# Performance work log

Hardware: AMD Instinct MI355X
Metric: run time of the kernel (lower is better)

## Reference

```python
import math
import jax, jax.numpy as jnp
import numpy as np

DIM = 96
HEADS = 3
HEAD_DIM = DIM // HEADS
WS = 8            # window_size
SHIFT = 4         # shift_size
N = WS * WS       # tokens per window
SCALE = HEAD_DIM ** (-0.5)


def _relative_positions_log():
    # matches WindowAttention.get_relative_positions (torch.meshgrid ij)
    coords = jnp.stack(jnp.meshgrid(jnp.arange(WS), jnp.arange(WS), indexing='ij'))  # [2,WS,WS]
    flat = coords.reshape(2, -1)                                # [2,N]
    rel = flat[:, :, None] - flat[:, None, :]                   # [2,N,N]
    rel = jnp.transpose(rel, (1, 2, 0)).astype(jnp.float32)     # [N,N,2]
    return jnp.sign(rel) * jnp.log1p(jnp.abs(rel))


def _conv1x1(x, w, b):
    # x: [B,C,H,W], w: [O,C], b: [O]
    return jnp.einsum('bchw,oc->bohw', x, w) + b[:, None, None]


def _conv3x3_reflect(x, w, b):
    # reflect padding=1, kernel 3x3
    xp = jnp.pad(x, ((0, 0), (0, 0), (1, 1), (1, 1)), mode='reflect')
    y = jax.lax.conv_general_dilated(xp, w, (1, 1), 'VALID',
                                     dimension_numbers=('NCHW', 'OIHW', 'NCHW'))
    return y + b[None, :, None, None]


def setup_inputs() -> dict:
    key = jax.random.key(0)
    ks = jax.random.split(key, 16)
    s = 0.02
    inp = {
        'x':      jax.random.normal(ks[0], (8, DIM, 256, 256), jnp.float32),
        'V_w':    jax.random.normal(ks[1], (DIM, DIM), jnp.float32) * s,
        'V_b':    jnp.zeros((DIM,), jnp.float32),
        'QK_w':   jax.random.normal(ks[2], (2 * DIM, DIM), jnp.float32) * s,
        'QK_b':   jnp.zeros((2 * DIM,), jnp.float32),
        'conv_w': jax.random.normal(ks[3], (DIM, DIM, 3, 3), jnp.float32) * s,
        'conv_b': jnp.zeros((DIM,), jnp.float32),
        'proj_w': jax.random.normal(ks[4], (DIM, DIM), jnp.float32) * s,
        'proj_b': jnp.zeros((DIM,), jnp.float32),
        'm1_w':   jax.random.normal(ks[5], (256, 2), jnp.float32) * 0.1,
        'm1_b':   jnp.zeros((256,), jnp.float32),
        'm2_w':   jax.random.normal(ks[6], (HEADS, 256), jnp.float32) * 0.1,
        'm2_b':   jnp.zeros((HEADS,), jnp.float32),
    }
    return inp


def reference(x, V_w, V_b, QK_w, QK_b, conv_w, conv_b, proj_w, proj_b,
              m1_w, m1_b, m2_w, m2_b):
    B, C, H, W = x.shape
    V = _conv1x1(x, V_w, V_b)                     # [B,C,H,W]
    QK = _conv1x1(x, QK_w, QK_b)                  # [B,2C,H,W]
    QKV = jnp.concatenate([QK, V], axis=1)        # [B,3C,H,W]

    # check_size with shift: H,W divisible by WS -> mod_pad = 0
    pad_r = (WS - SHIFT) % WS
    QKV = jnp.pad(QKV, ((0, 0), (0, 0), (SHIFT, pad_r), (SHIFT, pad_r)), mode='reflect')
    Ht, Wt = QKV.shape[2], QKV.shape[3]

    # window partition -> [B*nH*nW, N, 3C]
    sQ = jnp.transpose(QKV, (0, 2, 3, 1))         # [B,Ht,Wt,3C]
    nH, nW = Ht // WS, Wt // WS
    qkv = sQ.reshape(B, nH, WS, nW, WS, 3 * C)
    qkv = jnp.transpose(qkv, (0, 1, 3, 2, 4, 5)).reshape(-1, N, 3 * C)

    # window attention with MLP relative-position bias
    Bw = qkv.shape[0]
    qkv = qkv.reshape(Bw, N, 3, HEADS, HEAD_DIM)
    qkv = jnp.transpose(qkv, (2, 0, 3, 1, 4))     # [3,Bw,h,N,d]
    q, k, v = qkv[0], qkv[1], qkv[2]

    rel = _relative_positions_log()               # [N,N,2]
    hbias = jax.nn.gelu(rel @ m1_w.T + m1_b, approximate=False)
    bias = hbias @ m2_w.T + m2_b                  # [N,N,h]
    bias = jnp.transpose(bias, (2, 0, 1))         # [h,N,N]

    attn = jnp.einsum('bhnd,bhmd->bhnm', q, k) * SCALE + bias[None]
    attn = jax.nn.softmax(attn, axis=-1)
    xw = jnp.einsum('bhnm,bhmd->bhnd', attn, v)   # [Bw,h,N,d]
    xw = jnp.transpose(xw, (0, 2, 1, 3)).reshape(Bw, N, C)

    # window reverse -> [B,Ht,Wt,C]
    xr = xw.reshape(B, nH, nW, WS, WS, C)
    xr = jnp.transpose(xr, (0, 1, 3, 2, 4, 5)).reshape(B, Ht, Wt, C)
    attn_out = xr[:, SHIFT:SHIFT + H, SHIFT:SHIFT + W, :]
    attn_out = jnp.transpose(attn_out, (0, 3, 1, 2))   # [B,C,H,W]

    conv_out = _conv3x3_reflect(V, conv_w, conv_b)
    x_out = _conv1x1(conv_out + attn_out, proj_w, proj_b)
    return x_out
```

## Files before the change

kernel.cpp:

```cpp
#include <hip/hip_runtime.h>
#include <cstdint>

using u16 = unsigned short;
using u32 = unsigned int;
using f32x4  = __attribute__((ext_vector_type(4))) float;
using bf16x8 = __attribute__((ext_vector_type(8))) short;

#define NHEADS 3
#define WSZ 8
#define IMG 256
#define NPX 65536
#define NWIN 33
#define ATT_SCALE 0.17677669529663687f
#define INV_SCALE 5.656854249492381f
#define HALO_PITCH 104

__device__ __forceinline__ int refl(int i, int n) {
    return i < 0 ? -i : (i >= n ? 2*n - 2 - i : i);
}
__device__ __forceinline__ float bflo(u32 u){ union{u32 i; float f;} x; x.i = u << 16; return x.f; }
__device__ __forceinline__ float bfhi(u32 u){ union{u32 i; float f;} x; x.i = u & 0xffff0000u; return x.f; }
__device__ __forceinline__ float bf2f(u16 v){ union{u32 i; float f;} x; x.i = ((u32)v) << 16; return x.f; }
__device__ __forceinline__ u16 f2bf(float f){
    union{float f; u32 i;} x; x.f = f;
    u32 r = x.i + 0x7fffu + ((x.i >> 16) & 1u);
    return (u16)(r >> 16);
}
__device__ __forceinline__ u32 pk2bf(float a, float b){
    return (u32)f2bf(a) | ((u32)f2bf(b) << 16);
}

__global__ __launch_bounds__(256) void k_bias(
    const float* __restrict__ m1w, const float* __restrict__ m1b,
    const float* __restrict__ m2w, const float* __restrict__ m2b,
    float* __restrict__ biasS)
{
    int idx = blockIdx.x * 256 + threadIdx.x;
    int hh  = idx >> 12;
    int rem = idx & 4095;
    int n = rem >> 6, m = rem & 63;
    int di = (n >> 3) - (m >> 3);
    int dj = (n & 7)  - (m & 7);
    float fdi = copysignf(log1pf(fabsf((float)di)), (float)di);
    float fdj = copysignf(log1pf(fabsf((float)dj)), (float)dj);
    float acc = m2b[hh];
    for (int k = 0; k < 256; ++k) {
        float tv = fdi * m1w[2*k] + fdj * m1w[2*k+1] + m1b[k];
        float g  = 0.5f * tv * (1.0f + erff(tv * 0.70710678118654752f));
        acc = fmaf(g, m2w[hh*256 + k], acc);
    }
    biasS[hh*4096 + n*64 + m] = acc * INV_SCALE;
}

__global__ __launch_bounds__(64) void k_wprep(
    const float* __restrict__ cw, u16* __restrict__ Bfrag)
{
    int ks   = blockIdx.x;
    int lane = threadIdx.x;
    int nt    = ks % 6;
    int kstep = ks / 6;
    int tap   = kstep % 9;
    int ck    = kstep / 9;
    int dy = tap / 3, dx = tap % 3;
    int cout = nt*16 + (lane & 15);
    int cin0 = ck*32 + (lane >> 4)*8;
    u16* dst = Bfrag + (size_t)ks*512 + lane*8;
    #pragma unroll
    for (int j = 0; j < 8; ++j)
        dst[j] = f2bf(cw[((size_t)(cout*96 + cin0 + j))*9 + dy*3 + dx]);
}

__global__ __launch_bounds__(64) void k_wprep_qkv(
    const float* __restrict__ qkw, const float* __restrict__ vw,
    u16* __restrict__ BfragQ)
{
    int ks   = blockIdx.x;
    int lane = threadIdx.x;
    int nt    = ks % 18;
    int kstep = ks / 18;
    int o     = nt*16 + (lane & 15);
    int cin0  = kstep*32 + (lane >> 4)*8;
    const float* src = (o < 192) ? (qkw + (size_t)o*96 + cin0)
                                 : (vw + (size_t)(o - 192)*96 + cin0);
    u16* dst = BfragQ + (size_t)ks*512 + lane*8;
    #pragma unroll
    for (int j = 0; j < 8; ++j) dst[j] = f2bf(src[j]);
}

__global__ __launch_bounds__(64) void k_wprep_proj(
    const float* __restrict__ pw, u16* __restrict__ BfragP)
{
    int ks   = blockIdx.x;
    int lane = threadIdx.x;
    int nt    = ks % 6;
    int kstep = ks / 6;
    int o     = nt*16 + (lane & 15);
    int cin0  = kstep*32 + (lane >> 4)*8;
    u16* dst = BfragP + (size_t)ks*512 + lane*8;
    #pragma unroll
    for (int j = 0; j < 8; ++j) dst[j] = f2bf(pw[(size_t)o*96 + cin0 + j]);
}

__global__ __launch_bounds__(256, 2) void k_qkv(
    const float* __restrict__ x, const u16* __restrict__ BfragQ,
    const float* __restrict__ qkb, const float* __restrict__ vb,
    u16* __restrict__ qkv)
{
    int tile = blockIdx.x;
    int b    = tile >> 8;
    int pix0 = (tile & 255) * 256;
    size_t px0 = (size_t)tile * 256;
    int t    = threadIdx.x;

    __shared__ u16 xs[256 * HALO_PITCH];

    {
        const float* xb = x + (size_t)b*96*NPX + pix0 + t;
        u16* xrow = xs + t * HALO_PITCH;
        float v[96];
        #pragma unroll
        for (int c = 0; c < 96; ++c) v[c] = xb[(size_t)c * NPX];
        #pragma unroll
        for (int oct = 0; oct < 12; ++oct) {
            uint4 o;
            o.x = pk2bf(v[oct*8+0], v[oct*8+1]);
            o.y = pk2bf(v[oct*8+2], v[oct*8+3]);
            o.z = pk2bf(v[oct*8+4], v[oct*8+5]);
            o.w = pk2bf(v[oct*8+6], v[oct*8+7]);
            *(uint4*)(xrow + oct*8) = o;
        }
    }
    __syncthreads();

    int wv   = __builtin_amdgcn_readfirstlane(t >> 6);
    int lane = t & 63;
    int lc   = lane & 15;
    int kg   = lane >> 4;

    const u16* bbase = BfragQ + lane*8;

    #pragma unroll 1
    for (int og = 0; og < 3; ++og) {
        f32x4 acc[4][6] = {};
        #pragma unroll
        for (int kstep = 0; kstep < 3; ++kstep) {
            bf16x8 bF[6];
            #pragma unroll
            for (int nt = 0; nt < 6; ++nt)
                bF[nt] = *(const bf16x8*)(bbase + (size_t)(kstep*18 + og*6 + nt)*512);
            #pragma unroll
            for (int mt = 0; mt < 4; ++mt) {
                bf16x8 aF = *(const bf16x8*)(xs + (wv*64 + mt*16 + lc)*HALO_PITCH + kstep*32 + kg*8);
                #pragma unroll
                for (int nt = 0; nt < 6; ++nt)
                    acc[mt][nt] = __builtin_amdgcn_mfma_f32_16x16x32_bf16(aF, bF[nt], acc[mt][nt], 0, 0, 0);
            }
        }

        float bv[6];
        #pragma unroll
        for (int nt = 0; nt < 6; ++nt) {
            int o = og*96 + nt*16 + lc;
            bv[nt] = (o < 192) ? qkb[o] : vb[o - 192];
        }

        #pragma unroll
        for (int mt = 0; mt < 4; ++mt) {
            #pragma unroll
            for (int r = 0; r < 4; ++r) {
                size_t px = px0 + wv*64 + mt*16 + kg*4 + r;
                u16* qp = qkv + px*288 + og*96 + lc;
                #pragma unroll
                for (int nt = 0; nt < 6; ++nt)
                    qp[nt*16] = f2bf(acc[mt][nt][r] + bv[nt]);
            }
        }
    }
}

__global__ __launch_bounds__(256, 2) void k_attn(
    const u16* __restrict__ qkv, const float* __restrict__ biasS,
    u16* __restrict__ att)
{
    __shared__ u16 lds[27648];
    int t    = threadIdx.x;
    int wv   = __builtin_amdgcn_readfirstlane(t >> 6);
    int lane = t & 63;
    int lc   = lane & 15;
    int kg   = lane >> 4;

    u16* Plds = lds + wv * 6912;
    u16* Vlds = Plds + 4608;

    int win = blockIdx.x * 4 + wv;
    int b   = win / 1089;
    int wr  = win - b * 1089;
    int wy  = wr / NWIN;
    int wx  = wr - wy * NWIN;

    int py = wy*8 + (lane >> 3) - 4;
    int px = wx*8 + (lane & 7)  - 4;
    int iy = refl(py, IMG), ix = refl(px, IMG);
    int pxoff = b*NPX + iy*256 + ix;
    int vpx = (py >= 0 && py < IMG && px >= 0 && px < IMG) ? pxoff : (int)(pxoff | 0x80000000u);

    int pxA[4];
    #pragma unroll
    for (int mt = 0; mt < 4; ++mt)
        pxA[mt] = __builtin_amdgcn_ds_bpermute((16*mt + lc)*4, vpx) & 0x7fffffff;

    #pragma unroll 1
    for (int h = 0; h < 3; ++h) {
        {
            const u16* vrow = qkv + (size_t)pxoff*288 + 192 + h*32;
            #pragma unroll
            for (int g = 0; g < 4; ++g) {
                bf16x8 vv = *(const bf16x8*)(vrow + g*8);
                #pragma unroll
                for (int j = 0; j < 8; ++j)
                    Vlds[(g*8 + j)*72 + lane] = (u16)vv[j];
            }
        }

        bf16x8 afr[4], bfr[4];
        #pragma unroll
        for (int mt = 0; mt < 4; ++mt) {
            afr[mt] = *(const bf16x8*)(qkv + (size_t)pxA[mt]*288 + 96 + h*32 + kg*8);
            bfr[mt] = *(const bf16x8*)(qkv + (size_t)pxA[mt]*288 +      h*32 + kg*8);
        }

        f32x4 acc[4][4];
        const float* bb = biasS + h*4096 + lc*64 + 4*kg;
        #pragma unroll
        for (int nt = 0; nt < 4; ++nt)
            #pragma unroll
            for (int mt = 0; mt < 4; ++mt)
                acc[mt][nt] = *(const f32x4*)(bb + nt*1024 + mt*16);

        #pragma unroll
        for (int mt = 0; mt < 4; ++mt)
            #pragma unroll
            for (int nt = 0; nt < 4; ++nt)
                acc[mt][nt] = __builtin_amdgcn_mfma_f32_16x16x32_bf16(afr[mt], bfr[nt], acc[mt][nt], 0, 0, 0);

        #pragma unroll
        for (int nt = 0; nt < 4; ++nt) {
            float m = acc[0][nt][0];
            #pragma unroll
            for (int mt = 0; mt < 4; ++mt)
                #pragma unroll
                for (int r = 0; r < 4; ++r)
                    m = fmaxf(m, acc[mt][nt][r]);
            m = fmaxf(m, __shfl_xor(m, 16));
            m = fmaxf(m, __shfl_xor(m, 32));
            float s = 0.f;
            #pragma unroll
            for (int mt = 0; mt < 4; ++mt)
                #pragma unroll
                for (int r = 0; r < 4; ++r) {
                    float p = __expf((acc[mt][nt][r] - m) * ATT_SCALE);
                    acc[mt][nt][r] = p;
                    s += p;
                }
            s += __shfl_xor(s, 16);
            s += __shfl_xor(s, 32);
            float inv = 1.0f / s;
            #pragma unroll
            for (int mt = 0; mt < 4; ++mt)
                #pragma unroll
                for (int r = 0; r < 4; ++r)
                    acc[mt][nt][r] *= inv;
        }

        #pragma unroll
        for (int nt = 0; nt < 4; ++nt)
            #pragma unroll
            for (int mt = 0; mt < 4; ++mt) {
                uint2 pk;
                pk.x = pk2bf(acc[mt][nt][0], acc[mt][nt][1]);
                pk.y = pk2bf(acc[mt][nt][2], acc[mt][nt][3]);
                *(uint2*)(Plds + (16*nt + lc)*72 + 16*mt + 4*kg) = pk;
            }

        f32x4 oacc[4][2] = {};
        #pragma unroll
        for (int s = 0; s < 2; ++s) {
            bf16x8 vb2[2];
            #pragma unroll
            for (int ntpv = 0; ntpv < 2; ++ntpv)
                vb2[ntpv] = *(const bf16x8*)(Vlds + (16*ntpv + lc)*72 + s*32 + kg*8);
            #pragma unroll
            for (int mtpv = 0; mtpv < 4; ++mtpv) {
                bf16x8 pa = *(const bf16x8*)(Plds + (16*mtpv + lc)*72 + s*32 + kg*8);
                #pragma unroll
                for (int ntpv = 0; ntpv < 2; ++ntpv)
                    oacc[mtpv][ntpv] = __builtin_amdgcn_mfma_f32_16x16x32_bf16(pa, vb2[ntpv], oacc[mtpv][ntpv], 0, 0, 0);
            }
        }

        #pragma unroll
        for (int mtpv = 0; mtpv < 4; ++mtpv)
            #pragma unroll
            for (int rr = 0; rr < 4; ++rr) {
                int vp = __builtin_amdgcn_ds_bpermute((16*mtpv + 4*kg + rr)*4, vpx);
                if (vp >= 0) {
                    u16* op = att + (size_t)vp*96 + h*32 + lc;
                    op[0]  = f2bf(oacc[mtpv][0][rr]);
                    op[16] = f2bf(oacc[mtpv][1][rr]);
                }
            }
    }
}

__global__ __launch_bounds__(256, 2) void k_conv(
    const u16* __restrict__ qkv, const u16* __restrict__ att,
    const u16* __restrict__ Bfrag, const float* __restrict__ cb,
    u16* __restrict__ S)
{
    int tile = blockIdx.x;
    int b    = tile >> 8;
    int tr   = tile & 255;
    int ty0  = (tr >> 3) * 8;
    int tx0  = (tr & 7) * 32;
    int t    = threadIdx.x;

    __shared__ u16 vt[340 * HALO_PITCH];

    for (int p = t; p < 340; p += 256) {
        int hr = p / 34;
        int hc = p - hr * 34;
        int gy = refl(ty0 - 1 + hr, IMG);
        int gx = refl(tx0 - 1 + hc, IMG);
        const uint4* src = (const uint4*)(qkv + ((size_t)(b*NPX + gy*256 + gx))*288 + 192);
        uint4* dst = (uint4*)(vt + p * HALO_PITCH);
        #pragma unroll
        for (int q = 0; q < 12; ++q) dst[q] = src[q];
    }
    __syncthreads();

    int wv   = __builtin_amdgcn_readfirstlane(t >> 6);
    int lane = t & 63;
    int lc   = lane & 15;
    int kg   = lane >> 4;

    int abase[4];
    #pragma unroll
    for (int mt = 0; mt < 4; ++mt) {
        int r_mt = 2*wv + (mt >> 1);
        int c_mt = (mt & 1) * 16;
        abase[mt] = (r_mt*34 + c_mt + lc) * HALO_PITCH + kg*8;
    }

    f32x4 acc[4][6] = {};

    const u16* bfr = Bfrag + lane*8;
    #pragma unroll 1
    for (int ck = 0; ck < 3; ++ck) {
        const u16* bck = bfr + ck * 27648;
        int aoff = ck * 32;
        #pragma unroll
        for (int tap = 0; tap < 9; ++tap) {
            const int dy = tap / 3, dx = tap % 3;
            bf16x8 bF[6];
            #pragma unroll
            for (int nt = 0; nt < 6; ++nt)
                bF[nt] = *(const bf16x8*)(bck + (tap*6 + nt)*512);
            #pragma unroll
            for (int mt = 0; mt < 4; ++mt) {
                bf16x8 aF = *(const bf16x8*)(vt + abase[mt] + aoff + (dy*34 + dx)*HALO_PITCH);
                #pragma unroll
                for (int nt = 0; nt < 6; ++nt)
                    acc[mt][nt] = __builtin_amdgcn_mfma_f32_16x16x32_bf16(aF, bF[nt], acc[mt][nt], 0, 0, 0);
            }
        }
    }

    float cbv[6];
    #pragma unroll
    for (int nt = 0; nt < 6; ++nt) cbv[nt] = cb[nt*16 + lc];

    #pragma unroll
    for (int mt = 0; mt < 4; ++mt) {
        int r_mt = 2*wv + (mt >> 1);
        int c_mt = (mt & 1) * 16;
        int y    = ty0 + r_mt;
        #pragma unroll
        for (int r = 0; r < 4; ++r) {
            int x = tx0 + c_mt + kg*4 + r;
            size_t pbase = ((size_t)(b*NPX + y*256 + x))*96 + lc;
            #pragma unroll
            for (int nt = 0; nt < 6; ++nt) {
                float v = acc[mt][nt][r] + cbv[nt] + bf2f(att[pbase + nt*16]);
                S[pbase + nt*16] = f2bf(v);
            }
        }
    }
}

__global__ __launch_bounds__(256, 2) void k_proj(
    const u16* __restrict__ S, const u16* __restrict__ BfragP,
    const float* __restrict__ pb, float* __restrict__ out)
{
    int tile = blockIdx.x;
    int b    = tile >> 8;
    int pix0 = (tile & 255) * 256;
    size_t px0 = (size_t)tile * 256;
    int t    = threadIdx.x;
    int wv   = __builtin_amdgcn_readfirstlane(t >> 6);
    int lane = t & 63;
    int lc   = lane & 15;
    int kg   = lane >> 4;

    f32x4 acc[4][6] = {};
    const u16* arow  = S + (px0 + wv*64 + lc)*96 + kg*8;
    const u16* bbase = BfragP + lane*8;

    #pragma unroll
    for (int kstep = 0; kstep < 3; ++kstep) {
        bf16x8 bF[6];
        #pragma unroll
        for (int nt = 0; nt < 6; ++nt)
            bF[nt] = *(const bf16x8*)(bbase + (size_t)(kstep*6 + nt)*512);
        #pragma unroll
        for (int mt = 0; mt < 4; ++mt) {
            bf16x8 aF = *(const bf16x8*)(arow + (size_t)mt*16*96 + kstep*32);
            #pragma unroll
            for (int nt = 0; nt < 6; ++nt)
                acc[mt][nt] = __builtin_amdgcn_mfma_f32_16x16x32_bf16(aF, bF[nt], acc[mt][nt], 0, 0, 0);
        }
    }

    float bv[6];
    #pragma unroll
    for (int nt = 0; nt < 6; ++nt) bv[nt] = pb[nt*16 + lc];

    float* ob = out + (size_t)b*96*NPX;
    #pragma unroll
    for (int mt = 0; mt < 4; ++mt) {
        #pragma unroll
        for (int r = 0; r < 4; ++r) {
            int pxi = pix0 + wv*64 + mt*16 + kg*4 + r;
            #pragma unroll
            for (int nt = 0; nt < 6; ++nt)
                ob[(size_t)(nt*16 + lc)*NPX + pxi] = acc[mt][nt][r] + bv[nt];
        }
    }
}

extern "C" void kernel_launch(void* const* d_in, const int* in_sizes, int n_in,
                              void* d_out, int out_size, void* d_ws, size_t ws_size,
                              hipStream_t stream)
{
    const float* x      = (const float*)d_in[0];
    const float* V_w    = (const float*)d_in[1];
    const float* V_b    = (const float*)d_in[2];
    const float* QK_w   = (const float*)d_in[3];
    const float* QK_b   = (const float*)d_in[4];
    const float* conv_w = (const float*)d_in[5];
    const float* conv_b = (const float*)d_in[6];
    const float* proj_w = (const float*)d_in[7];
    const float* proj_b = (const float*)d_in[8];
    const float* m1_w   = (const float*)d_in[9];
    const float* m1_b   = (const float*)d_in[10];
    const float* m2_w   = (const float*)d_in[11];
    const float* m2_b   = (const float*)d_in[12];
    float* out = (float*)d_out;

    char* ws = (char*)d_ws;
    float* biasS = (float*)ws;
    u16* qkvb = (u16*)(ws + 49152);
    u16* attb = (u16*)(ws + 49152 + 301989888);
    u16* sbuf = (u16*)(ws + 49152 + 301989888 + 100663296);

    char* ob = (char*)d_out;
    u16* Bfrag  = (u16*)ob;
    u16* BfragQ = (u16*)(ob + (1 << 20));
    u16* BfragP = (u16*)attb;

    hipLaunchKernelGGL(k_wprep,      dim3(162),     dim3(64),  0, stream, conv_w, Bfrag);
    hipLaunchKernelGGL(k_wprep_qkv,  dim3(54),      dim3(64),  0, stream, QK_w, V_w, BfragQ);
    hipLaunchKernelGGL(k_bias,       dim3(48),      dim3(256), 0, stream, m1_w, m1_b, m2_w, m2_b, biasS);
    hipLaunchKernelGGL(k_qkv,        dim3(2048),    dim3(256), 0, stream, x, BfragQ, QK_b, V_b, qkvb);
    hipLaunchKernelGGL(k_attn,       dim3(2178),    dim3(256), 0, stream, qkvb, biasS, attb);
    hipLaunchKernelGGL(k_conv,       dim3(2048),    dim3(256), 0, stream, qkvb, attb, Bfrag, conv_b, sbuf);
    hipLaunchKernelGGL(k_wprep_proj, dim3(18),      dim3(64),  0, stream, proj_w, BfragP);
    hipLaunchKernelGGL(k_proj,       dim3(2048),    dim3(256), 0, stream, sbuf, BfragP, proj_b, out);
}
```

Before: 591.7 us.

## Fuse 3x3 conv and 1x1 projection into one kernel via LDS staging

After: 523.8 us. -11.5%, faster.

```diff
diff --git a/kernel.cpp b/kernel.cpp
--- a/kernel.cpp
+++ b/kernel.cpp
@@ -312,10 +312,11 @@
     }
 }
 
-__global__ __launch_bounds__(256, 2) void k_conv(
+__global__ __launch_bounds__(256, 2) void k_convproj(
     const u16* __restrict__ qkv, const u16* __restrict__ att,
     const u16* __restrict__ Bfrag, const float* __restrict__ cb,
-    u16* __restrict__ S)
+    const u16* __restrict__ BfragP, const float* __restrict__ pb,
+    float* __restrict__ out)
 {
     int tile = blockIdx.x;
     int b    = tile >> 8;
@@ -379,6 +380,8 @@
     #pragma unroll
     for (int nt = 0; nt < 6; ++nt) cbv[nt] = cb[nt*16 + lc];
 
+    __syncthreads();
+
     #pragma unroll
     for (int mt = 0; mt < 4; ++mt) {
         int r_mt = 2*wv + (mt >> 1);
@@ -386,35 +389,21 @@
         int y    = ty0 + r_mt;
         #pragma unroll
         for (int r = 0; r < 4; ++r) {
-            int x = tx0 + c_mt + kg*4 + r;
+            int x  = tx0 + c_mt + kg*4 + r;
+            int pl = r_mt*32 + c_mt + kg*4 + r;
             size_t pbase = ((size_t)(b*NPX + y*256 + x))*96 + lc;
+            u16* srow = vt + pl * HALO_PITCH + lc;
             #pragma unroll
             for (int nt = 0; nt < 6; ++nt) {
                 float v = acc[mt][nt][r] + cbv[nt] + bf2f(att[pbase + nt*16]);
-                S[pbase + nt*16] = f2bf(v);
-            }
-        }
-    }
-}
-
-__global__ __launch_bounds__(256, 2) void k_proj(
-    const u16* __restrict__ S, const u16* __restrict__ BfragP,
-    const float* __restrict__ pb, float* __restrict__ out)
-{
-    int tile = blockIdx.x;
-    int b    = tile >> 8;
-    int pix0 = (tile & 255) * 256;
-    size_t px0 = (size_t)tile * 256;
-    int t    = threadIdx.x;
-    int wv   = __builtin_amdgcn_readfirstlane(t >> 6);
-    int lane = t & 63;
-    int lc   = lane & 15;
-    int kg   = lane >> 4;
-
-    f32x4 acc[4][6] = {};
-    const u16* arow  = S + (px0 + wv*64 + lc)*96 + kg*8;
+                srow[nt*16] = f2bf(v);
+            }
+        }
+    }
+    __syncthreads();
+
+    f32x4 pacc[4][6] = {};
     const u16* bbase = BfragP + lane*8;
-
     #pragma unroll
     for (int kstep = 0; kstep < 3; ++kstep) {
         bf16x8 bF[6];
@@ -423,10 +412,10 @@
             bF[nt] = *(const bf16x8*)(bbase + (size_t)(kstep*6 + nt)*512);
         #pragma unroll
         for (int mt = 0; mt < 4; ++mt) {
-            bf16x8 aF = *(const bf16x8*)(arow + (size_t)mt*16*96 + kstep*32);
+            bf16x8 aF = *(const bf16x8*)(vt + (wv*64 + mt*16 + lc)*HALO_PITCH + kstep*32 + kg*8);
             #pragma unroll
             for (int nt = 0; nt < 6; ++nt)
-                acc[mt][nt] = __builtin_amdgcn_mfma_f32_16x16x32_bf16(aF, bF[nt], acc[mt][nt], 0, 0, 0);
+                pacc[mt][nt] = __builtin_amdgcn_mfma_f32_16x16x32_bf16(aF, bF[nt], pacc[mt][nt], 0, 0, 0);
         }
     }
 
@@ -439,10 +428,12 @@
     for (int mt = 0; mt < 4; ++mt) {
         #pragma unroll
         for (int r = 0; r < 4; ++r) {
-            int pxi = pix0 + wv*64 + mt*16 + kg*4 + r;
+            int pl = wv*64 + mt*16 + kg*4 + r;
+            int y  = ty0 + (pl >> 5);
+            int x  = tx0 + (pl & 31);
             #pragma unroll
             for (int nt = 0; nt < 6; ++nt)
-                ob[(size_t)(nt*16 + lc)*NPX + pxi] = acc[mt][nt][r] + bv[nt];
+                ob[(size_t)(nt*16 + lc)*NPX + y*256 + x] = pacc[mt][nt][r] + bv[nt];
         }
     }
 }
@@ -470,19 +461,17 @@
     float* biasS = (float*)ws;
     u16* qkvb = (u16*)(ws + 49152);
     u16* attb = (u16*)(ws + 49152 + 301989888);
-    u16* sbuf = (u16*)(ws + 49152 + 301989888 + 100663296);
-
-    char* ob = (char*)d_out;
-    u16* Bfrag  = (u16*)ob;
-    u16* BfragQ = (u16*)(ob + (1 << 20));
-    u16* BfragP = (u16*)attb;
+    char* scr = ws + 49152 + 301989888 + 100663296;
+
+    u16* Bfrag  = (u16*)scr;
+    u16* BfragQ = (u16*)(scr + (1 << 20));
+    u16* BfragP = (u16*)(scr + (2 << 20));
 
     hipLaunchKernelGGL(k_wprep,      dim3(162),     dim3(64),  0, stream, conv_w, Bfrag);
     hipLaunchKernelGGL(k_wprep_qkv,  dim3(54),      dim3(64),  0, stream, QK_w, V_w, BfragQ);
+    hipLaunchKernelGGL(k_wprep_proj, dim3(18),      dim3(64),  0, stream, proj_w, BfragP);
     hipLaunchKernelGGL(k_bias,       dim3(48),      dim3(256), 0, stream, m1_w, m1_b, m2_w, m2_b, biasS);
     hipLaunchKernelGGL(k_qkv,        dim3(2048),    dim3(256), 0, stream, x, BfragQ, QK_b, V_b, qkvb);
     hipLaunchKernelGGL(k_attn,       dim3(2178),    dim3(256), 0, stream, qkvb, biasS, attb);
-    hipLaunchKernelGGL(k_conv,       dim3(2048),    dim3(256), 0, stream, qkvb, attb, Bfrag, conv_b, sbuf);
-    hipLaunchKernelGGL(k_wprep_proj, dim3(18),      dim3(64),  0, stream, proj_w, BfragP);
-    hipLaunchKernelGGL(k_proj,       dim3(2048),    dim3(256), 0, stream, sbuf, BfragP, proj_b, out);
-}
+    hipLaunchKernelGGL(k_convproj,   dim3(2048),    dim3(256), 0, stream, qkvb, attb, Bfrag, conv_b, BfragP, proj_b, out);
+}
```
